# Optimization experiments

Measured on AMD Instinct MI355X. Metric: run time of the kernel, lower is better.

## Reference

```python
import jax, jax.numpy as jnp
import numpy as np


def _conv(x, w, b, stride):
    # x: [B,C,H,W], w: [O,I,3,3], padding=1, given stride
    y = jax.lax.conv_general_dilated(
        x, w, window_strides=(stride, stride), padding=((1, 1), (1, 1)),
        dimension_numbers=("NCHW", "OIHW", "NCHW"))
    return y + b[None, :, None, None]


def setup_inputs() -> dict:
    key = jax.random.key(0)
    ks = jax.random.split(key, 9)
    B, H, W = 16, 256, 256
    hidden, vocab = 768, 8192
    c1, c2 = hidden // 4, hidden // 2

    def he(k, shape, fan_in):
        return jax.random.normal(k, shape, dtype=jnp.float32) * (1.0 / np.sqrt(fan_in))

    return {
        "image": jax.random.normal(ks[0], (B, 3, H, W), dtype=jnp.float32),
        "w1": he(ks[1], (c1, 3, 3, 3), 3 * 9),
        "b1": jnp.zeros((c1,), jnp.float32),
        "w2": he(ks[2], (c2, c1, 3, 3), c1 * 9),
        "b2": jnp.zeros((c2,), jnp.float32),
        "w3": he(ks[3], (hidden, c2, 3, 3), c2 * 9),
        "b3": jnp.zeros((hidden,), jnp.float32),
        "codebook": jax.random.normal(ks[4], (vocab, hidden), dtype=jnp.float32),
        "embedding_table": jax.random.normal(ks[5], (vocab, hidden), dtype=jnp.float32),
        "resolution_level": 0,
    }


def reference(image, w1, b1, w2, b2, w3, b3, codebook, embedding_table, resolution_level):
    # conv encoder: 3 -> C/4 -> C/2 -> C, each stride 2 (spatial /8)
    f = jax.nn.relu(_conv(image, w1, b1, 2))
    f = jax.nn.relu(_conv(f, w2, b2, 2))
    f = _conv(f, w3, b3, 2)                      # [B,C,H',W']
    B, C, Hp, Wp = f.shape
    feats = f.reshape(B, C, Hp * Wp).transpose(0, 2, 1)  # [B, HW, C]

    # squared euclidean distances to codebook (argmin invariant under sqrt)
    f2 = jnp.sum(feats * feats, axis=-1, keepdims=True)          # [B,HW,1]
    c2 = jnp.sum(codebook * codebook, axis=-1)                   # [V]
    d2 = f2 - 2.0 * jnp.einsum("bnc,vc->bnv", feats, codebook) + c2  # [B,HW,V]
    tokens = jnp.argmin(d2, axis=-1)                             # [B,HW] int
    embeddings = embedding_table[tokens]                         # [B,HW,C]
    return tokens, embeddings
```

## Files before the change

### kernel.cpp

```cpp
#include <hip/hip_runtime.h>
#include <hip/hip_bf16.h>
#include <float.h>


typedef __attribute__((ext_vector_type(4))) float f32x4;
typedef __attribute__((ext_vector_type(8))) _Float16 f16x8;
typedef __attribute__((ext_vector_type(8))) unsigned short u16x8;

__device__ __forceinline__ void split_f16(float x, unsigned short& hb, unsigned short& lb) {
    _Float16 h = (_Float16)x;
    _Float16 l = (_Float16)(x - (float)h);
    hb = __builtin_bit_cast(unsigned short, h);
    lb = __builtin_bit_cast(unsigned short, l);
}

__device__ __forceinline__ void gload16(const void* g, const unsigned short* l) {
    typedef unsigned int __attribute__((address_space(1))) g_u32;
    typedef unsigned int __attribute__((address_space(3))) l_u32;
    __builtin_amdgcn_global_load_lds((const g_u32*)g, (l_u32*)l, 16, 0, 0);
}

__global__ __launch_bounds__(256) void zero_kernel(unsigned short* z) {
    u16x8 v = {0, 0, 0, 0, 0, 0, 0, 0};
    *(u16x8*)&z[threadIdx.x * 8] = v;
}

__global__ __launch_bounds__(256) void reorder_w_kernel(
    const float* __restrict__ w, unsigned short* __restrict__ wh,
    unsigned short* __restrict__ wl, int COUT, int CIN)
{
    const int t = blockIdx.x * 256 + threadIdx.x;
    const int c8n = CIN / 8;
    const int total = COUT * 9 * c8n;
    if (t >= total) return;
    const int c8 = t % c8n;
    const int tap = (t / c8n) % 9;
    const int o = t / (9 * c8n);
    u16x8 vh, vl;
#pragma unroll
    for (int k = 0; k < 8; ++k) {
        const int c = c8 * 8 + k;
        unsigned short hb, lb;
        split_f16(w[((size_t)o * CIN + c) * 9 + tap], hb, lb);
        vh[k] = hb; vl[k] = lb;
    }
    const size_t dst = ((size_t)o * 9 + tap) * CIN + c8 * 8;
    *(u16x8*)&wh[dst] = vh;
    *(u16x8*)&wl[dst] = vl;
}

template <int CIN, int COUT, int HIN, int HOUT>
__global__ __launch_bounds__(256) void conv1_direct(
    const float* __restrict__ in,
    const float* __restrict__ w, const float* __restrict__ bias,
    unsigned short* __restrict__ ah, unsigned short* __restrict__ al, int nb)
{
    constexpr int WIN = HIN, WOUT = HOUT;
    constexpr int NXT = WOUT / 4;
    constexpr int NOT = COUT / 8;
    int t = blockIdx.x * 256 + threadIdx.x;
    const int total = nb * NOT * HOUT * NXT;
    if (t >= total) return;

    const int xt = t % NXT;
    const int y  = (t / NXT) % HOUT;
    int ot = (t / (NXT * HOUT)) % NOT;
    int bl = t / (NXT * HOUT * NOT);
    ot = __builtin_amdgcn_readfirstlane(ot);
    bl = __builtin_amdgcn_readfirstlane(bl);

    const int x0 = xt * 4, o0 = ot * 8;
    float acc[8][4];
#pragma unroll
    for (int i = 0; i < 8; ++i) {
        float bv = bias[o0 + i];
#pragma unroll
        for (int j = 0; j < 4; ++j) acc[i][j] = bv;
    }

    const float* inb = in + (size_t)bl * CIN * HIN * WIN;
    const float* wb  = w + (size_t)o0 * CIN * 9;

    for (int c = 0; c < CIN; ++c) {
        const float* inc = inb + (size_t)c * HIN * WIN;
#pragma unroll
        for (int ky = 0; ky < 3; ++ky) {
            const int iy = 2 * y - 1 + ky;
            if ((unsigned)iy < (unsigned)HIN) {
                const float* row = inc + (size_t)iy * WIN;
                const int sx0 = 2 * x0 - 1;
                float xin[9];
                xin[0] = (sx0 >= 0) ? row[sx0] : 0.f;
#pragma unroll
                for (int k = 1; k < 9; ++k) xin[k] = row[sx0 + k];
#pragma unroll
                for (int i = 0; i < 8; ++i) {
                    const float* wr = wb + ((size_t)i * CIN + c) * 9 + ky * 3;
                    const float w0 = wr[0], w1 = wr[1], w2 = wr[2];
#pragma unroll
                    for (int j = 0; j < 4; ++j)
                        acc[i][j] = fmaf(w0, xin[2 * j],
                                    fmaf(w1, xin[2 * j + 1],
                                    fmaf(w2, xin[2 * j + 2], acc[i][j])));
                }
            }
        }
    }

#pragma unroll
    for (int j = 0; j < 4; ++j) {
        u16x8 vh, vl;
#pragma unroll
        for (int i = 0; i < 8; ++i) {
            unsigned short hb, lb;
            split_f16(fmaxf(acc[i][j], 0.f), hb, lb);
            vh[i] = hb; vl[i] = lb;
        }
        const size_t m = (size_t)bl * (HOUT * WOUT) + (size_t)y * WOUT + x0 + j;
        *(u16x8*)&ah[m * COUT + o0] = vh;
        *(u16x8*)&al[m * COUT + o0] = vl;
    }
}

template <int CIN, int COUT, int HIN, int HOUT, int LOGW, int LOGHW, bool RELU>
__global__ __launch_bounds__(256) void conv_gemm(
    const unsigned short* __restrict__ inh, const unsigned short* __restrict__ inl,
    const unsigned short* __restrict__ wrh, const unsigned short* __restrict__ wrl,
    const float* __restrict__ bias,
    unsigned short* __restrict__ outh, unsigned short* __restrict__ outl,
    const unsigned short* __restrict__ zeros)
{
    constexpr int WIN = HIN, WOUT = HOUT;
    constexpr int KCPT = CIN / 64;
    constexpr int NSTEP = 9 * KCPT;

    __shared__ unsigned short lds[32768];
    unsigned short* As_h = lds;
    unsigned short* As_l = lds + 8192;
    unsigned short* Bs_h = lds + 16384;
    unsigned short* Bs_l = lds + 24576;

    const int tid  = threadIdx.x;
    const int lane = tid & 63;
    const int wid  = tid >> 6;
    const int ntile = blockIdx.x, mtile = blockIdx.y;
    const int m0 = mtile * 128, n0 = ntile * 128;
    const int wm = wid >> 1, wn = wid & 1;

    int aoff0[4], boff0[4], yv[4], xv[4], dstb[4];
#pragma unroll
    for (int p = 0; p < 4; ++p) {
        const int s = wid * 64 + p * 256 + lane;
        const int r = s >> 3;
        const int cl = (s & 7) ^ (r & 7);
        const int m = m0 + r;
        const int b = m >> LOGHW;
        const int y = (m >> LOGW) & (HOUT - 1);
        const int x = m & (WOUT - 1);
        yv[p] = y; xv[p] = x;
        aoff0[p] = ((b * HIN + 2 * y) * WIN + 2 * x) * CIN + cl * 8;
        boff0[p] = (n0 + r) * 9 * CIN + cl * 8;
        dstb[p] = (wid * 64 + p * 256) * 8;
    }

    f32x4 acc[4][4];
#pragma unroll
    for (int i = 0; i < 4; ++i)
#pragma unroll
        for (int j = 0; j < 4; ++j) acc[i][j] = f32x4{0.f, 0.f, 0.f, 0.f};

    for (int ks = 0; ks < NSTEP; ++ks) {
        const int tap = ks / KCPT;
        const int c0 = (ks % KCPT) * 64;
        const int ky = tap / 3, kx = tap - ky * 3;
        const int doff = ((ky - 1) * WIN + (kx - 1)) * CIN + c0;

#pragma unroll
        for (int p = 0; p < 4; ++p) {
            const bool valid = !((yv[p] == 0 && ky == 0) || (xv[p] == 0 && kx == 0));
            const unsigned short* sa_h = valid ? inh + (aoff0[p] + doff) : zeros;
            const unsigned short* sa_l = valid ? inl + (aoff0[p] + doff) : zeros;
            gload16(sa_h, As_h + dstb[p]);
            gload16(sa_l, As_l + dstb[p]);
            const int bo = boff0[p] + tap * CIN + c0;
            gload16(wrh + bo, Bs_h + dstb[p]);
            gload16(wrl + bo, Bs_l + dstb[p]);
        }
        __syncthreads();

#pragma unroll
        for (int kh = 0; kh < 2; ++kh) {
            const int cg = kh * 4 + (lane >> 4);
            f16x8 a_h[4], a_l[4], b_h[4], b_l[4];
#pragma unroll
            for (int i = 0; i < 4; ++i) {
                const int row = wm * 64 + i * 16 + (lane & 15);
                const int off = row * 64 + ((cg ^ (row & 7)) * 8);
                a_h[i] = *(const f16x8*)(As_h + off);
                a_l[i] = *(const f16x8*)(As_l + off);
            }
#pragma unroll
            for (int j = 0; j < 4; ++j) {
                const int col = wn * 64 + j * 16 + (lane & 15);
                const int off = col * 64 + ((cg ^ (col & 7)) * 8);
                b_h[j] = *(const f16x8*)(Bs_h + off);
                b_l[j] = *(const f16x8*)(Bs_l + off);
            }
            __builtin_amdgcn_s_setprio(1);
#pragma unroll
            for (int i = 0; i < 4; ++i)
#pragma unroll
                for (int j = 0; j < 4; ++j) {
                    acc[i][j] = __builtin_amdgcn_mfma_f32_16x16x32_f16(
                        a_h[i], b_h[j], acc[i][j], 0, 0, 0);
                    acc[i][j] = __builtin_amdgcn_mfma_f32_16x16x32_f16(
                        a_h[i], b_l[j], acc[i][j], 0, 0, 0);
                    acc[i][j] = __builtin_amdgcn_mfma_f32_16x16x32_f16(
                        a_l[i], b_h[j], acc[i][j], 0, 0, 0);
                }
            __builtin_amdgcn_s_setprio(0);
        }
        __syncthreads();
    }

    float bv4[4];
#pragma unroll
    for (int j = 0; j < 4; ++j) bv4[j] = bias[n0 + wn * 64 + j * 16 + (lane & 15)];
#pragma unroll
    for (int i = 0; i < 4; ++i)
#pragma unroll
        for (int r = 0; r < 4; ++r) {
            const size_t m = m0 + wm * 64 + i * 16 + (lane >> 4) * 4 + r;
#pragma unroll
            for (int j = 0; j < 4; ++j) {
                const int n = n0 + wn * 64 + j * 16 + (lane & 15);
                float v = acc[i][j][r] + bv4[j];
                if (RELU) v = fmaxf(v, 0.f);
                unsigned short hb, lb;
                split_f16(v, hb, lb);
                outh[m * COUT + n] = hb;
                outl[m * COUT + n] = lb;
            }
        }
}

__global__ __launch_bounds__(256) void split_codebook_kernel(
    const float* __restrict__ cb, unsigned short* __restrict__ bh,
    unsigned short* __restrict__ bl, float* __restrict__ c2)
{
    const int v = blockIdx.x * 4 + (threadIdx.x >> 6);
    const int lane = threadIdx.x & 63;
    const float* row = cb + (size_t)v * 768;
    float s = 0.f;
#pragma unroll
    for (int t = 0; t < 12; ++t) {
        const int idx = lane + 64 * t;
        float x = row[idx];
        s = fmaf(x, x, s);
        unsigned short hb, lb;
        split_f16(x, hb, lb);
        bh[(size_t)v * 768 + idx] = hb;
        bl[(size_t)v * 768 + idx] = lb;
    }
#pragma unroll
    for (int off = 32; off >= 1; off >>= 1) s += __shfl_xor(s, off, 64);
    if (lane == 0) c2[v] = s;
}

__global__ __launch_bounds__(256) void vq_mfma_kernel(
    const unsigned short* __restrict__ Ah, const unsigned short* __restrict__ Al,
    const unsigned short* __restrict__ Bh, const unsigned short* __restrict__ Bl,
    const float* __restrict__ c2,
    float* __restrict__ pval, int* __restrict__ pidx)
{
    __shared__ unsigned short lds[32768];
    unsigned short* As_h = lds;
    unsigned short* As_l = lds + 8192;
    unsigned short* Bs_h = lds + 16384;
    unsigned short* Bs_l = lds + 24576;

    const int tid  = threadIdx.x;
    const int lane = tid & 63;
    const int wid  = tid >> 6;

    const int bid    = blockIdx.x;
    const int xcd    = bid & 7;
    const int local  = bid >> 3;
    const int msuper = local >> 5;
    const int idx5   = local & 31;
    const int mtile  = msuper * 4 + (idx5 & 3);
    const int ntile  = xcd * 8 + (idx5 >> 2);

    const int m0 = mtile * 128, n0 = ntile * 128;
    const int wm = wid >> 1, wn = wid & 1;

    f32x4 acc[4][4];
#pragma unroll
    for (int i = 0; i < 4; ++i)
#pragma unroll
        for (int j = 0; j < 4; ++j) acc[i][j] = f32x4{0.f, 0.f, 0.f, 0.f};

    for (int step = 0; step < 12; ++step) {
        const int kb = step * 64;
#pragma unroll
        for (int p = 0; p < 4; ++p) {
            const int s  = wid * 64 + p * 256 + lane;
            const int r  = s >> 3;
            const int cl = (s & 7) ^ (r & 7);
            const int dstbase = (wid * 64 + p * 256) * 8;
            const size_t ga = (size_t)(m0 + r) * 768 + kb + cl * 8;
            const size_t gb = (size_t)(n0 + r) * 768 + kb + cl * 8;
            gload16(Ah + ga, As_h + dstbase);
            gload16(Al + ga, As_l + dstbase);
            gload16(Bh + gb, Bs_h + dstbase);
            gload16(Bl + gb, Bs_l + dstbase);
        }
        __syncthreads();

#pragma unroll
        for (int kh = 0; kh < 2; ++kh) {
            const int cg = kh * 4 + (lane >> 4);
            f16x8 a_h[4], a_l[4], b_h[4], b_l[4];
#pragma unroll
            for (int i = 0; i < 4; ++i) {
                const int row = wm * 64 + i * 16 + (lane & 15);
                const int off = row * 64 + ((cg ^ (row & 7)) * 8);
                a_h[i] = *(const f16x8*)(As_h + off);
                a_l[i] = *(const f16x8*)(As_l + off);
            }
#pragma unroll
            for (int j = 0; j < 4; ++j) {
                const int col = wn * 64 + j * 16 + (lane & 15);
                const int off = col * 64 + ((cg ^ (col & 7)) * 8);
                b_h[j] = *(const f16x8*)(Bs_h + off);
                b_l[j] = *(const f16x8*)(Bs_l + off);
            }
            __builtin_amdgcn_s_setprio(1);
#pragma unroll
            for (int i = 0; i < 4; ++i)
#pragma unroll
                for (int j = 0; j < 4; ++j) {
                    acc[i][j] = __builtin_amdgcn_mfma_f32_16x16x32_f16(
                        a_h[i], b_h[j], acc[i][j], 0, 0, 0);
                    acc[i][j] = __builtin_amdgcn_mfma_f32_16x16x32_f16(
                        a_h[i], b_l[j], acc[i][j], 0, 0, 0);
                    acc[i][j] = __builtin_amdgcn_mfma_f32_16x16x32_f16(
                        a_l[i], b_h[j], acc[i][j], 0, 0, 0);
                }
            __builtin_amdgcn_s_setprio(0);
        }
        __syncthreads();
    }

    float bestv[4][4];
    int   besti[4][4];
#pragma unroll
    for (int i = 0; i < 4; ++i)
#pragma unroll
        for (int r = 0; r < 4; ++r) { bestv[i][r] = FLT_MAX; besti[i][r] = 0; }

#pragma unroll
    for (int j = 0; j < 4; ++j) {
        const int n = n0 + wn * 64 + j * 16 + (lane & 15);
        const float cn = c2[n];
#pragma unroll
        for (int i = 0; i < 4; ++i)
#pragma unroll
            for (int r = 0; r < 4; ++r) {
                float val = fmaf(-2.f, acc[i][j][r], cn);
                if (val < bestv[i][r] || (val == bestv[i][r] && n < besti[i][r])) {
                    bestv[i][r] = val; besti[i][r] = n;
                }
            }
    }

    const int chunk = ntile * 2 + wn;
#pragma unroll
    for (int i = 0; i < 4; ++i)
#pragma unroll
        for (int r = 0; r < 4; ++r) {
            float v = bestv[i][r];
            int  ix = besti[i][r];
#pragma unroll
            for (int off = 8; off >= 1; off >>= 1) {
                float ov = __shfl_xor(v, off, 64);
                int   oi = __shfl_xor(ix, off, 64);
                if (ov < v || (ov == v && oi < ix)) { v = ov; ix = oi; }
            }
            if ((lane & 15) == 0) {
                const int m = m0 + wm * 64 + i * 16 + (lane >> 4) * 4 + r;
                pval[(size_t)chunk * 16384 + m] = v;
                pidx[(size_t)chunk * 16384 + m] = ix;
            }
        }
}

__global__ __launch_bounds__(256) void token_reduce_kernel(
    const float* __restrict__ pval, const int* __restrict__ pidx,
    float* __restrict__ tok_out)
{
    const int m = blockIdx.x * 256 + threadIdx.x;
    float bv = pval[m];
    int   bi = pidx[m];
    for (int c = 1; c < 128; ++c) {
        float v = pval[(size_t)c * 16384 + m];
        int   i = pidx[(size_t)c * 16384 + m];
        if (v < bv || (v == bv && i < bi)) { bv = v; bi = i; }
    }
    tok_out[m] = (float)bi;
}

__global__ __launch_bounds__(192) void gather_kernel(
    const float* __restrict__ tok, const float* __restrict__ table,
    float* __restrict__ emb)
{
    const int m = blockIdx.x;
    const int t = threadIdx.x;
    const int token = (int)tok[m];
    const float4* src = (const float4*)(table + (size_t)token * 768);
    float4* dst = (float4*)(emb + (size_t)m * 768);
    dst[t] = src[t];
}

extern "C" void kernel_launch(void* const* d_in, const int* in_sizes, int n_in,
                              void* d_out, int out_size, void* d_ws, size_t ws_size,
                              hipStream_t stream)
{
    const float* image = (const float*)d_in[0];
    const float* w1 = (const float*)d_in[1];
    const float* b1 = (const float*)d_in[2];
    const float* w2 = (const float*)d_in[3];
    const float* b2 = (const float*)d_in[4];
    const float* w3 = (const float*)d_in[5];
    const float* b3 = (const float*)d_in[6];
    const float* codebook = (const float*)d_in[7];
    const float* etab     = (const float*)d_in[8];

    float* out_tok = (float*)d_out;
    float* out_emb = (float*)d_out + 16384;

    char* ws = (char*)d_ws;
    unsigned short* Ah  = (unsigned short*)ws;
    unsigned short* Al  = (unsigned short*)(ws + 25165824);
    unsigned short* f1h = (unsigned short*)(ws + 50331648);
    unsigned short* f1l = (unsigned short*)(ws + 75497472);
    unsigned short* Bh  = (unsigned short*)(ws + 50331648);
    unsigned short* Bl  = (unsigned short*)(ws + 62914560);
    float* c2   = (float*)(ws + 75497472);
    float* pval = (float*)(ws + 75530240);
    int*   pidx = (int*)  (ws + 83918848);
    unsigned short* f2h = (unsigned short*)(ws + 100663296);
    unsigned short* f2l = (unsigned short*)(ws + 113246208);
    unsigned short* wr2h = (unsigned short*)(ws + 125829120);
    unsigned short* wr2l = (unsigned short*)(ws + 127156224);
    unsigned short* wr3h = (unsigned short*)(ws + 128483328);
    unsigned short* wr3l = (unsigned short*)(ws + 133791744);
    unsigned short* zeros = (unsigned short*)(ws + 139100160);

    zero_kernel<<<1, 256, 0, stream>>>(zeros);
    reorder_w_kernel<<<(384 * 9 * 24 + 255) / 256, 256, 0, stream>>>(w2, wr2h, wr2l, 384, 192);
    reorder_w_kernel<<<(768 * 9 * 48 + 255) / 256, 256, 0, stream>>>(w3, wr3h, wr3l, 768, 384);

    for (int bc = 0; bc < 4; ++bc) {
        const int b0 = bc * 4;
        const int total1 = 4 * (192 / 8) * 128 * (128 / 4);
        conv1_direct<3, 192, 256, 128>
            <<<total1 / 256, 256, 0, stream>>>(
                image + (size_t)b0 * 3 * 256 * 256, w1, b1, f1h, f1l, 4);
        conv_gemm<192, 384, 128, 64, 6, 12, true>
            <<<dim3(3, 128), 256, 0, stream>>>(
                f1h, f1l, wr2h, wr2l, b2, f2h, f2l, zeros);
        conv_gemm<384, 768, 64, 32, 5, 10, false>
            <<<dim3(6, 32), 256, 0, stream>>>(
                f2h, f2l, wr3h, wr3l, b3,
                Ah + (size_t)b0 * 1024 * 768, Al + (size_t)b0 * 1024 * 768, zeros);
    }

    split_codebook_kernel<<<2048, 256, 0, stream>>>(codebook, Bh, Bl, c2);

    vq_mfma_kernel<<<8192, 256, 0, stream>>>(Ah, Al, Bh, Bl, c2, pval, pidx);

    token_reduce_kernel<<<64, 256, 0, stream>>>(pval, pidx, out_tok);

    gather_kernel<<<16384, 192, 0, stream>>>(out_tok, etab, out_emb);
}
```

Before: 1.500 ms.

## Batch conv stages into larger chunks and run conv3 once over all images

When the workspace is large enough, a new memory layout is used. conv1 and conv2 run over chunks of 8 (or 4) images with the f2 output kept for the whole batch, and conv3 then runs as a single launch over all 16 images. This cuts launch count and gives each conv launch more blocks, which should improve occupancy on a wide GPU. It depends on ws_size, so if the harness workspace is smaller the old path still runs.

```diff
diff --git a/kernel.cpp b/kernel.cpp
--- a/kernel.cpp
+++ b/kernel.cpp
@@ -440,6 +440,59 @@
     float* out_emb = (float*)d_out + 16384;
 
     char* ws = (char*)d_ws;
+
+    const bool big = ws_size >= 214601728ull;
+    const bool mid = !big && ws_size >= 164270080ull;
+
+    if (big || mid) {
+        const size_t F1PL = big ? 50331648ull : 25165824ull;
+        const size_t F2OFF = 2 * F1PL;
+        const size_t WOFF  = F2OFF + 100663296ull;
+
+        unsigned short* f1h = (unsigned short*)ws;
+        unsigned short* f1l = (unsigned short*)(ws + F1PL);
+        unsigned short* Ah  = (unsigned short*)ws;
+        unsigned short* Al  = (unsigned short*)(ws + 25165824);
+        unsigned short* f2h = (unsigned short*)(ws + F2OFF);
+        unsigned short* f2l = (unsigned short*)(ws + F2OFF + 50331648);
+        unsigned short* Bh  = (unsigned short*)(ws + F2OFF);
+        unsigned short* Bl  = (unsigned short*)(ws + F2OFF + 12582912);
+        float* c2   = (float*)(ws + F2OFF + 25165824);
+        float* pval = (float*)(ws + F2OFF + 25198592);
+        int*   pidx = (int*)  (ws + F2OFF + 33587200);
+        unsigned short* wr2h = (unsigned short*)(ws + WOFF);
+        unsigned short* wr2l = (unsigned short*)(ws + WOFF + 1327104);
+        unsigned short* wr3h = (unsigned short*)(ws + WOFF + 2654208);
+        unsigned short* wr3l = (unsigned short*)(ws + WOFF + 7962624);
+        unsigned short* zeros = (unsigned short*)(ws + WOFF + 13271040);
+
+        zero_kernel<<<1, 256, 0, stream>>>(zeros);
+        reorder_w_kernel<<<(384 * 9 * 24 + 255) / 256, 256, 0, stream>>>(w2, wr2h, wr2l, 384, 192);
+        reorder_w_kernel<<<(768 * 9 * 48 + 255) / 256, 256, 0, stream>>>(w3, wr3h, wr3l, 768, 384);
+
+        const int nbc = big ? 2 : 4;
+        const int nbi = big ? 8 : 4;
+        for (int bc = 0; bc < nbc; ++bc) {
+            const int b0 = bc * nbi;
+            const int total1 = nbi * (192 / 8) * 128 * (128 / 4);
+            conv1_direct<3, 192, 256, 128>
+                <<<total1 / 256, 256, 0, stream>>>(
+                    image + (size_t)b0 * 3 * 256 * 256, w1, b1, f1h, f1l, nbi);
+            conv_gemm<192, 384, 128, 64, 6, 12, true>
+                <<<dim3(3, nbi * 32), 256, 0, stream>>>(
+                    f1h, f1l, wr2h, wr2l, b2,
+                    f2h + (size_t)b0 * 4096 * 384, f2l + (size_t)b0 * 4096 * 384, zeros);
+        }
+        conv_gemm<384, 768, 64, 32, 5, 10, false>
+            <<<dim3(6, 128), 256, 0, stream>>>(f2h, f2l, wr3h, wr3l, b3, Ah, Al, zeros);
+
+        split_codebook_kernel<<<2048, 256, 0, stream>>>(codebook, Bh, Bl, c2);
+        vq_mfma_kernel<<<8192, 256, 0, stream>>>(Ah, Al, Bh, Bl, c2, pval, pidx);
+        token_reduce_kernel<<<64, 256, 0, stream>>>(pval, pidx, out_tok);
+        gather_kernel<<<16384, 192, 0, stream>>>(out_tok, etab, out_emb);
+        return;
+    }
+
     unsigned short* Ah  = (unsigned short*)ws;
     unsigned short* Al  = (unsigned short*)(ws + 25165824);
     unsigned short* f1h = (unsigned short*)(ws + 50331648);
@@ -477,10 +530,7 @@
     }
 
     split_codebook_kernel<<<2048, 256, 0, stream>>>(codebook, Bh, Bl, c2);
-
     vq_mfma_kernel<<<8192, 256, 0, stream>>>(Ah, Al, Bh, Bl, c2, pval, pidx);
-
     token_reduce_kernel<<<64, 256, 0, stream>>>(pval, pidx, out_tok);
-
     gather_kernel<<<16384, 192, 0, stream>>>(out_tok, etab, out_emb);
 }
```

Result: faster. 1.279 ms (median of 2 runs) (-14.7%).
